# Performance work log

Hardware: AMD Instinct MI355X
Metric: run time of the kernel (lower is better)

The kernel has to match this reference:

```python
import jax, jax.numpy as jnp
import numpy as np
import math

D_MODEL = 256
D_HIDDEN = 64
NUM_HEADS = 4
LN_EPS = 1e-5


def _layernorm(x, gamma, beta):
    mu = jnp.mean(x, axis=-1, keepdims=True)
    var = jnp.mean(jnp.square(x - mu), axis=-1, keepdims=True)
    return (x - mu) * jax.lax.rsqrt(var + LN_EPS) * gamma + beta


def setup_inputs() -> dict:
    key = jax.random.key(0)
    ks = jax.random.split(key, 12)
    B, T, Nt, Nw = 8, 96, 200, 100
    s = 0.02
    return {
        "turbine_feats": jax.random.normal(ks[0], (B, T, Nt, D_MODEL), jnp.float32),
        "weather_feats": jax.random.normal(ks[1], (B, T, Nw, D_MODEL), jnp.float32),
        # torch Linear layout: (out_features, in_features)
        "w_t_lin": jax.random.normal(ks[2], (D_HIDDEN, D_MODEL), jnp.float32) * s,
        "b_t_lin": jnp.zeros((D_HIDDEN,), jnp.float32),
        "w_w_lin": jax.random.normal(ks[3], (D_HIDDEN, D_MODEL), jnp.float32) * s,
        "b_w_lin": jnp.zeros((D_HIDDEN,), jnp.float32),
        "ln_t_g": jnp.ones((D_HIDDEN,), jnp.float32),
        "ln_t_b": jnp.zeros((D_HIDDEN,), jnp.float32),
        "ln_w_g": jnp.ones((D_HIDDEN,), jnp.float32),
        "ln_w_b": jnp.zeros((D_HIDDEN,), jnp.float32),
        # nn.MultiheadAttention packed qkv in_proj (3*dh, dh) + out_proj
        "in_proj_w": jax.random.normal(ks[4], (3 * D_HIDDEN, D_HIDDEN), jnp.float32) * s,
        "in_proj_b": jnp.zeros((3 * D_HIDDEN,), jnp.float32),
        "attn_out_w": jax.random.normal(ks[5], (D_HIDDEN, D_HIDDEN), jnp.float32) * s,
        "attn_out_b": jnp.zeros((D_HIDDEN,), jnp.float32),
        "out_proj_w": jax.random.normal(ks[6], (D_MODEL, D_HIDDEN), jnp.float32) * s,
        "out_proj_b": jnp.zeros((D_MODEL,), jnp.float32),
    }


def reference(turbine_feats, weather_feats, w_t_lin, b_t_lin, w_w_lin, b_w_lin,
              ln_t_g, ln_t_b, ln_w_g, ln_w_b, in_proj_w, in_proj_b,
              attn_out_w, attn_out_b, out_proj_w, out_proj_b):
    B, T, Nt, C = turbine_feats.shape
    Nw = weather_feats.shape[2]
    dh, H = D_HIDDEN, NUM_HEADS
    hd = dh // H

    # project + layernorm
    h_t = _layernorm(jnp.einsum('btnc,dc->btnd', turbine_feats, w_t_lin) + b_t_lin, ln_t_g, ln_t_b)
    h_w = _layernorm(jnp.einsum('btmc,dc->btmd', weather_feats, w_w_lin) + b_w_lin, ln_w_g, ln_w_b)

    # hand-rolled turbine->weather cross attention
    logits = jnp.einsum('btnd,btmd->btnm', h_t, h_w) / math.sqrt(dh)  # [B,T,Nt,Nw]
    attn = jax.nn.softmax(logits, axis=-1)
    context = jnp.einsum('btnm,btmd->btnd', attn, h_w)  # [B,T,Nt,dh]

    # nn.MultiheadAttention self-attention over turbines, per (B,T)
    x = context.reshape(B * T, Nt, dh)
    wq, wk, wv = in_proj_w[:dh], in_proj_w[dh:2 * dh], in_proj_w[2 * dh:]
    bq, bk, bv = in_proj_b[:dh], in_proj_b[dh:2 * dh], in_proj_b[2 * dh:]
    q = (jnp.einsum('snd,ed->sne', x, wq) + bq).reshape(B * T, Nt, H, hd)
    k = (jnp.einsum('snd,ed->sne', x, wk) + bk).reshape(B * T, Nt, H, hd)
    v = (jnp.einsum('snd,ed->sne', x, wv) + bv).reshape(B * T, Nt, H, hd)
    scores = jnp.einsum('snhd,smhd->shnm', q, k) / math.sqrt(hd)  # [BT,H,Nt,Nt]
    w = jax.nn.softmax(scores, axis=-1)
    o = jnp.einsum('shnm,smhd->snhd', w, v).reshape(B * T, Nt, dh)
    o = jnp.einsum('snd,ed->sne', o, attn_out_w) + attn_out_b

    enhanced = o.reshape(B, T, Nt, dh)
    return turbine_feats + jnp.einsum('btnd,cd->btnc', enhanced, out_proj_w) + out_proj_b
```

## Files before the change

kernel.cpp:

```cpp
#include <hip/hip_runtime.h>


#define DEV __device__ __forceinline__

typedef float  f32x4  __attribute__((ext_vector_type(4)));
typedef int    i32x4  __attribute__((ext_vector_type(4)));
typedef unsigned int u32x2 __attribute__((ext_vector_type(2)));
typedef __bf16 bf16x8 __attribute__((ext_vector_type(8)));

DEV f32x4 mfma_bf16(i32x4 a, i32x4 b, f32x4 c) {
  return __builtin_amdgcn_mfma_f32_16x16x32_bf16(
      __builtin_bit_cast(bf16x8, a), __builtin_bit_cast(bf16x8, b), c, 0, 0, 0);
}

DEV unsigned short f2b(float f) {
  unsigned int u = __builtin_bit_cast(unsigned int, f);
  u += 0x7FFFu + ((u >> 16) & 1u);
  return (unsigned short)(u >> 16);
}

__global__ void cvt_weights_k(const float* __restrict__ w0, const float* __restrict__ w1,
                              const float* __restrict__ w2, const float* __restrict__ w3,
                              const float* __restrict__ w4, unsigned short* __restrict__ out) {
  int i = blockIdx.x * 256 + threadIdx.x;
  int idx = i;
  float v;
  if (idx < 16384) v = w0[idx];
  else if ((idx -= 16384) < 16384) v = w1[idx];
  else if ((idx -= 16384) < 12288) v = w2[idx];
  else if ((idx -= 12288) < 4096)  v = w3[idx];
  else { idx -= 4096; if (idx >= 16384) return; v = w4[idx]; }
  out[i] = f2b(v);
}

template <int CIN, int COUT, int MODE, bool F32IN>
__global__ __launch_bounds__(256) void affine_k(
    const void* __restrict__ xin,
    const unsigned short* __restrict__ Wb,
    const float* __restrict__ bias,
    const float* __restrict__ gamma, const float* __restrict__ beta,
    void* __restrict__ outp) {
  const int tid = threadIdx.x;
  const long row0 = (long)blockIdx.x * 64;
  const int lane = tid & 63, wv = tid >> 6;
  const int m = lane & 15, quad = lane >> 4;
  const long grow = row0 + wv * 16 + m;

  constexpr int KS = CIN / 32;
  i32x4 a_reg[KS];
  if (F32IN) {
    const float* xf = (const float*)xin + grow * CIN + quad * 8;
    float4 v0[KS], v1[KS];
#pragma unroll
    for (int ks = 0; ks < KS; ++ks) {
      v0[ks] = *(const float4*)(xf + ks * 32);
      v1[ks] = *(const float4*)(xf + ks * 32 + 4);
    }
#pragma unroll
    for (int ks = 0; ks < KS; ++ks) {
      unsigned int p0 = (unsigned int)f2b(v0[ks].x) | ((unsigned int)f2b(v0[ks].y) << 16);
      unsigned int p1 = (unsigned int)f2b(v0[ks].z) | ((unsigned int)f2b(v0[ks].w) << 16);
      unsigned int p2 = (unsigned int)f2b(v1[ks].x) | ((unsigned int)f2b(v1[ks].y) << 16);
      unsigned int p3 = (unsigned int)f2b(v1[ks].z) | ((unsigned int)f2b(v1[ks].w) << 16);
      a_reg[ks] = (i32x4){(int)p0, (int)p1, (int)p2, (int)p3};
    }
  } else {
    const unsigned short* xb = (const unsigned short*)xin + grow * CIN + quad * 8;
#pragma unroll
    for (int ks = 0; ks < KS; ++ks)
      a_reg[ks] = *(const i32x4*)(xb + ks * 32);
  }

  if (MODE == 1) {
    float accs[4][4];
#pragma unroll
    for (int ct = 0; ct < 4; ++ct) {
      f32x4 acc = {0.f, 0.f, 0.f, 0.f};
      const unsigned short* wp = Wb + (ct * 16 + m) * CIN + quad * 8;
#pragma unroll
      for (int ks = 0; ks < KS; ++ks) {
        i32x4 b = *(const i32x4*)(wp + ks * 32);
        acc = mfma_bf16(a_reg[ks], b, acc);
      }
      float bv = bias[ct * 16 + m];
#pragma unroll
      for (int rg = 0; rg < 4; ++rg) accs[ct][rg] = acc[rg] + bv;
    }
    float g[4], bb[4];
#pragma unroll
    for (int ct = 0; ct < 4; ++ct) { g[ct] = gamma[ct * 16 + m]; bb[ct] = beta[ct * 16 + m]; }
    unsigned short* ob = (unsigned short*)outp;
#pragma unroll
    for (int rg = 0; rg < 4; ++rg) {
      float s = accs[0][rg] + accs[1][rg] + accs[2][rg] + accs[3][rg];
#pragma unroll
      for (int msk = 1; msk < 16; msk <<= 1) s += __shfl_xor(s, msk, 64);
      float mu = s * (1.0f / 64.0f);
      float vs = 0.f;
#pragma unroll
      for (int ct = 0; ct < 4; ++ct) { float d = accs[ct][rg] - mu; vs += d * d; }
#pragma unroll
      for (int msk = 1; msk < 16; msk <<= 1) vs += __shfl_xor(vs, msk, 64);
      float inv = rsqrtf(vs * (1.0f / 64.0f) + 1e-5f);
      long row = row0 + wv * 16 + quad * 4 + rg;
#pragma unroll
      for (int ct = 0; ct < 4; ++ct) {
        float y = (accs[ct][rg] - mu) * inv * g[ct] + bb[ct];
        ob[row * 64 + ct * 16 + m] = f2b(y);
      }
    }
  } else {
#pragma unroll
    for (int ct = 0; ct < COUT / 16; ++ct) {
      f32x4 acc = {0.f, 0.f, 0.f, 0.f};
      const unsigned short* wp = Wb + (ct * 16 + m) * CIN + quad * 8;
#pragma unroll
      for (int ks = 0; ks < KS; ++ks) {
        i32x4 b = *(const i32x4*)(wp + ks * 32);
        acc = mfma_bf16(a_reg[ks], b, acc);
      }
      int col = ct * 16 + m;
      float bv = bias[col];
      unsigned short* ob = (unsigned short*)outp;
#pragma unroll
      for (int rg = 0; rg < 4; ++rg) {
        long row = row0 + wv * 16 + quad * 4 + rg;
        ob[row * COUT + col] = f2b(acc[rg] + bv);
      }
    }
  }
}

__global__ __launch_bounds__(256) void out_fused_k(
    const unsigned short* __restrict__ o,
    const unsigned short* __restrict__ Wao,
    const float* __restrict__ bao,
    const unsigned short* __restrict__ Wop,
    const float* __restrict__ bop,
    const float* __restrict__ resid,
    float* __restrict__ out) {
  __shared__ __align__(16) unsigned short xs[64][72];
  __shared__ __align__(16) unsigned short as[64][72];
  __shared__ __align__(16) float Ls[4][16][68];
  const int tid = threadIdx.x;
  const long row0 = (long)blockIdx.x * 64;

  {
    const i32x4* xb = (const i32x4*)o + (size_t)row0 * 8;
    for (int i = tid; i < 512; i += 256) {
      int r = i >> 3, c = i & 7;
      *(i32x4*)&xs[r][c * 8] = xb[i];
    }
  }
  __syncthreads();

  const int lane = tid & 63, wv = tid >> 6;
  const int m = lane & 15, quad = lane >> 4;
  const int arow = wv * 16 + m;

  i32x4 af0 = *(const i32x4*)&xs[arow][quad * 8];
  i32x4 af1 = *(const i32x4*)&xs[arow][32 + quad * 8];

#pragma unroll
  for (int ct = 0; ct < 4; ++ct) {
    const unsigned short* wp = Wao + (ct * 16 + m) * 64 + quad * 8;
    f32x4 acc = {0.f, 0.f, 0.f, 0.f};
    acc = mfma_bf16(af0, *(const i32x4*)wp, acc);
    acc = mfma_bf16(af1, *(const i32x4*)(wp + 32), acc);
    float bv = bao[ct * 16 + m];
#pragma unroll
    for (int rg = 0; rg < 4; ++rg)
      as[wv * 16 + quad * 4 + rg][ct * 16 + m] = f2b(acc[rg] + bv);
  }
  __builtin_amdgcn_s_waitcnt(0);

  i32x4 bf0 = *(const i32x4*)&as[arow][quad * 8];
  i32x4 bf1 = *(const i32x4*)&as[arow][32 + quad * 8];

  const float4* residv = (const float4*)resid;
  float4* outv = (float4*)out;

  size_t gibase[4];
#pragma unroll
  for (int i = 0; i < 4; ++i) {
    int idx = lane + i * 64;
    int r = idx >> 4, c4 = idx & 15;
    gibase[i] = (size_t)(row0 + wv * 16 + r) * 64 + c4;
  }

#pragma unroll
  for (int cg = 0; cg < 4; ++cg) {
    float4 rv[4];
#pragma unroll
    for (int i = 0; i < 4; ++i) rv[i] = residv[gibase[i] + cg * 16];

#pragma unroll
    for (int c2 = 0; c2 < 4; ++c2) {
      int col = cg * 64 + c2 * 16 + m;
      const unsigned short* wp = Wop + col * 64 + quad * 8;
      f32x4 acc = {0.f, 0.f, 0.f, 0.f};
      acc = mfma_bf16(bf0, *(const i32x4*)wp, acc);
      acc = mfma_bf16(bf1, *(const i32x4*)(wp + 32), acc);
      float bv = bop[col];
#pragma unroll
      for (int rg = 0; rg < 4; ++rg)
        Ls[wv][quad * 4 + rg][c2 * 16 + m] = acc[rg] + bv;
    }
    __builtin_amdgcn_s_waitcnt(0);
#pragma unroll
    for (int i = 0; i < 4; ++i) {
      int idx = lane + i * 64;
      int r = idx >> 4, c4 = idx & 15;
      f32x4 sv = *(const f32x4*)&Ls[wv][r][c4 * 4];
      float4 ov;
      ov.x = sv[0] + rv[i].x; ov.y = sv[1] + rv[i].y;
      ov.z = sv[2] + rv[i].z; ov.w = sv[3] + rv[i].w;
      outv[gibase[i] + cg * 16] = ov;
    }
    __builtin_amdgcn_s_waitcnt(0);
  }
}

__global__ __launch_bounds__(256) void cross_attn_k(
    const unsigned short* __restrict__ ht,
    const unsigned short* __restrict__ hw,
    unsigned short* __restrict__ xout) {
  const int bt = blockIdx.x;
  const int tid = threadIdx.x;
  __shared__ __align__(16) unsigned short Kl[112][72];
  __shared__ __align__(16) unsigned short VT2[64][136];
  __shared__ __align__(16) unsigned short P2[4][16][136];

  const i32x4 z4 = {0, 0, 0, 0};
  {
    i32x4* p0 = (i32x4*)&Kl[0][0];
    for (int i = tid; i < 1008; i += 256) p0[i] = z4;
    i32x4* p1 = (i32x4*)&VT2[0][0];
    for (int i = tid; i < 1088; i += 256) p1[i] = z4;
    i32x4* p2 = (i32x4*)&P2[0][0][0];
    for (int i = tid; i < 1088; i += 256) p2[i] = z4;
  }
  __syncthreads();
  {
    const unsigned short* wbase = hw + (size_t)bt * 100 * 64;
    for (int i = tid; i < 800; i += 256) {
      int r = i >> 3, c = (i & 7) * 8;
      i32x4 w = *(const i32x4*)(wbase + (size_t)r * 64 + c);
      *(i32x4*)&Kl[r][c] = w;
      unsigned short tmp[8];
      __builtin_memcpy(tmp, &w, 16);
#pragma unroll
      for (int j = 0; j < 8; ++j) VT2[c + j][r] = tmp[j];
    }
  }
  __syncthreads();

  const int lane = tid & 63, wv = tid >> 6;
  const int m = lane & 15, quad = lane >> 4;

  i32x4 kf[7][2];
#pragma unroll
  for (int mt = 0; mt < 7; ++mt)
#pragma unroll
    for (int ks = 0; ks < 2; ++ks)
      kf[mt][ks] = *(const i32x4*)&Kl[mt * 16 + m][ks * 32 + quad * 8];

  for (int c = wv; c < 13; c += 4) {
    const int n0 = c * 16;
    const unsigned short* ap = ht + ((size_t)bt * 200 + n0 + m) * 64 + quad * 8;
    i32x4 a0 = *(const i32x4*)ap;
    i32x4 a1 = *(const i32x4*)(ap + 32);

    float s[7][4];
#pragma unroll
    for (int mt = 0; mt < 7; ++mt) {
      f32x4 acc = mfma_bf16(a0, kf[mt][0], (f32x4){0.f, 0.f, 0.f, 0.f});
      acc = mfma_bf16(a1, kf[mt][1], acc);
#pragma unroll
      for (int rg = 0; rg < 4; ++rg) s[mt][rg] = acc[rg];
    }
#pragma unroll
    for (int rg = 0; rg < 4; ++rg)
      s[6][rg] = (m < 4) ? s[6][rg] : -3.0e38f;

    float S[4];
#pragma unroll
    for (int rg = 0; rg < 4; ++rg) {
      float mx = s[0][rg];
#pragma unroll
      for (int mt = 1; mt < 7; ++mt) mx = fmaxf(mx, s[mt][rg]);
#pragma unroll
      for (int msk = 1; msk < 16; msk <<= 1) mx = fmaxf(mx, __shfl_xor(mx, msk, 64));
      float sum = 0.f;
#pragma unroll
      for (int mt = 0; mt < 7; ++mt) {
        float p = __expf((s[mt][rg] - mx) * 0.125f);
        s[mt][rg] = p; sum += p;
      }
#pragma unroll
      for (int msk = 1; msk < 16; msk <<= 1) sum += __shfl_xor(sum, msk, 64);
      S[rg] = sum;
    }
#pragma unroll
    for (int mt = 0; mt < 7; ++mt)
#pragma unroll
      for (int rg = 0; rg < 4; ++rg)
        P2[wv][quad * 4 + rg][mt * 16 + m] = f2b(s[mt][rg]);
    __builtin_amdgcn_s_waitcnt(0);

    i32x4 pa[4];
#pragma unroll
    for (int ks = 0; ks < 4; ++ks)
      pa[ks] = *(const i32x4*)&P2[wv][m][ks * 32 + quad * 8];
    float rs[4];
#pragma unroll
    for (int rg = 0; rg < 4; ++rg) rs[rg] = __fdividef(1.0f, S[rg]);

#pragma unroll
    for (int ct = 0; ct < 4; ++ct) {
      f32x4 acc = {0.f, 0.f, 0.f, 0.f};
#pragma unroll
      for (int ks = 0; ks < 4; ++ks) {
        i32x4 b = *(const i32x4*)&VT2[ct * 16 + m][ks * 32 + quad * 8];
        acc = mfma_bf16(pa[ks], b, acc);
      }
#pragma unroll
      for (int rg = 0; rg < 4; ++rg) {
        int n = n0 + quad * 4 + rg;
        if (n < 200)
          xout[((size_t)bt * 200 + n) * 64 + ct * 16 + m] = f2b(acc[rg] * rs[rg]);
      }
    }
  }
}

__global__ __launch_bounds__(256) void self_attn_k(
    const unsigned short* __restrict__ qkv,
    unsigned short* __restrict__ o) {
  const int g = blockIdx.x;
  const int bt = ((g >> 5) << 3) | (g & 7);
  const int h = (g >> 3) & 3;
  const int tid = threadIdx.x;

  __shared__ __align__(16) unsigned short Kz[212][24];
  __shared__ __align__(16) unsigned short VT[16][232];
  __shared__ __align__(16) unsigned short P[4][16][232];

  const i32x4 z4 = {0, 0, 0, 0};
  {
    i32x4* p0 = (i32x4*)&Kz[0][0];
    for (int i = tid; i < 636; i += 256) p0[i] = z4;
    i32x4* p1 = (i32x4*)&VT[0][0];
    for (int i = tid; i < 464; i += 256) p1[i] = z4;
    i32x4* p2 = (i32x4*)&P[0][0][0];
    for (int i = tid; i < 1856; i += 256) p2[i] = z4;
  }
  __syncthreads();
  {
    const unsigned short* kb = qkv + (size_t)bt * 200 * 192 + 64 + h * 16;
    const unsigned short* vb = kb + 64;
    for (int i = tid; i < 400; i += 256) {
      int r = i >> 1, c = (i & 1) * 8;
      *(i32x4*)&Kz[r][c] = *(const i32x4*)(kb + (size_t)r * 192 + c);
      i32x4 vv = *(const i32x4*)(vb + (size_t)r * 192 + c);
      unsigned short tmp[8];
      __builtin_memcpy(tmp, &vv, 16);
#pragma unroll
      for (int j = 0; j < 8; ++j) VT[c + j][r] = tmp[j];
    }
  }
  __syncthreads();

  const int lane = tid & 63, wv = tid >> 6;
  const int m = lane & 15, quad = lane >> 4;
  const bool kreal = quad < 2;

  i32x4 kf[13];
#pragma unroll
  for (int mt = 0; mt < 13; ++mt)
    kf[mt] = *(const i32x4*)&Kz[mt * 16 + m][quad * 8];

  const unsigned short* qb = qkv + (size_t)bt * 200 * 192 + h * 16;

  for (int c = wv; c < 13; c += 4) {
    const int n0 = c * 16;
    i32x4 a = kreal ? *(const i32x4*)(qb + (size_t)(n0 + m) * 192 + quad * 8) : z4;

    float s[13][4];
#pragma unroll
    for (int mt = 0; mt < 13; ++mt) {
      f32x4 acc = mfma_bf16(a, kf[mt], (f32x4){0.f, 0.f, 0.f, 0.f});
#pragma unroll
      for (int rg = 0; rg < 4; ++rg) s[mt][rg] = acc[rg];
    }
#pragma unroll
    for (int rg = 0; rg < 4; ++rg)
      s[12][rg] = (m < 8) ? s[12][rg] : -3.0e38f;

    float S[4];
#pragma unroll
    for (int rg = 0; rg < 4; ++rg) {
      float mx = s[0][rg];
#pragma unroll
      for (int mt = 1; mt < 13; ++mt) mx = fmaxf(mx, s[mt][rg]);
#pragma unroll
      for (int msk = 1; msk < 16; msk <<= 1) mx = fmaxf(mx, __shfl_xor(mx, msk, 64));
      float sum = 0.f;
#pragma unroll
      for (int mt = 0; mt < 13; ++mt) {
        float p = __expf((s[mt][rg] - mx) * 0.25f);
        s[mt][rg] = p; sum += p;
      }
#pragma unroll
      for (int msk = 1; msk < 16; msk <<= 1) sum += __shfl_xor(sum, msk, 64);
      S[rg] = sum;
    }
#pragma unroll
    for (int mt = 0; mt < 13; ++mt)
#pragma unroll
      for (int rg = 0; rg < 4; ++rg)
        P[wv][quad * 4 + rg][mt * 16 + m] = f2b(s[mt][rg]);
    __builtin_amdgcn_s_waitcnt(0);

    f32x4 acc2 = {0.f, 0.f, 0.f, 0.f};
#pragma unroll
    for (int ks = 0; ks < 7; ++ks) {
      i32x4 pa = *(const i32x4*)&P[wv][m][ks * 32 + quad * 8];
      i32x4 vb2 = *(const i32x4*)&VT[m][ks * 32 + quad * 8];
      acc2 = mfma_bf16(pa, vb2, acc2);
    }
#pragma unroll
    for (int rg = 0; rg < 4; ++rg) {
      int n = n0 + quad * 4 + rg;
      if (n < 200)
        o[((size_t)bt * 200 + n) * 64 + h * 16 + m] = f2b(__fdividef(acc2[rg], S[rg]));
    }
  }
}

extern "C" void kernel_launch(void* const* d_in, const int* in_sizes, int n_in,
                              void* d_out, int out_size, void* d_ws, size_t ws_size,
                              hipStream_t stream) {
  const float* turbine    = (const float*)d_in[0];
  const float* weather    = (const float*)d_in[1];
  const float* b_t_lin    = (const float*)d_in[3];
  const float* b_w_lin    = (const float*)d_in[5];
  const float* ln_t_g     = (const float*)d_in[6];
  const float* ln_t_b     = (const float*)d_in[7];
  const float* ln_w_g     = (const float*)d_in[8];
  const float* ln_w_b     = (const float*)d_in[9];
  const float* in_proj_b  = (const float*)d_in[11];
  const float* attn_out_b = (const float*)d_in[13];
  const float* out_proj_b = (const float*)d_in[15];

  unsigned short* ws  = (unsigned short*)d_ws;
  unsigned short* ht  = ws + 0;
  unsigned short* hw  = ws + 9830400;
  unsigned short* x   = ws + 14745600;
  unsigned short* qkv = ws + 24576000;
  unsigned short* o   = ws + 0;
  unsigned short* wb  = ws + 54067200;
  unsigned short* wtb = wb;
  unsigned short* wwb = wb + 16384;
  unsigned short* ipb = wb + 32768;
  unsigned short* aob = wb + 45056;
  unsigned short* opb = wb + 49152;

  cvt_weights_k<<<256, 256, 0, stream>>>((const float*)d_in[2], (const float*)d_in[4],
                                         (const float*)d_in[10], (const float*)d_in[12],
                                         (const float*)d_in[14], wb);
  affine_k<256, 64, 1, true><<<2400, 256, 0, stream>>>(
      turbine, wtb, b_t_lin, ln_t_g, ln_t_b, ht);
  affine_k<256, 64, 1, true><<<1200, 256, 0, stream>>>(
      weather, wwb, b_w_lin, ln_w_g, ln_w_b, hw);
  cross_attn_k<<<768, 256, 0, stream>>>(ht, hw, x);
  affine_k<64, 192, 0, false><<<2400, 256, 0, stream>>>(
      x, ipb, in_proj_b, nullptr, nullptr, qkv);
  self_attn_k<<<3072, 256, 0, stream>>>(qkv, o);
  out_fused_k<<<2400, 256, 0, stream>>>(
      o, aob, attn_out_b, opb, out_proj_b, turbine, (float*)d_out);
}
```

Before: 557.6 us.

## Fuse QKV in-projection into cross-attention kernel with head-major QKV layout

The cross-attention kernel now keeps its context tile in LDS and applies the packed QKV in-projection directly. This removes the separate affine kernel launch and the write and read of the intermediate context tensor. QKV is written in a head-major layout (per bt, per head, rows of 48) so self-attention loads its K and V with contiguous reads. The cost is more LDS per block (the larger PQ buffer plus XT) and more serial work per wave inside the cross kernel, which may reduce occupancy.

```diff
diff --git a/kernel.cpp b/kernel.cpp
--- a/kernel.cpp
+++ b/kernel.cpp
@@ -33,13 +33,13 @@
   out[i] = f2b(v);
 }
 
-template <int CIN, int COUT, int MODE, bool F32IN>
-__global__ __launch_bounds__(256) void affine_k(
-    const void* __restrict__ xin,
+template <int CIN>
+__global__ __launch_bounds__(256) void ln_affine_k(
+    const float* __restrict__ xin,
     const unsigned short* __restrict__ Wb,
     const float* __restrict__ bias,
     const float* __restrict__ gamma, const float* __restrict__ beta,
-    void* __restrict__ outp) {
+    unsigned short* __restrict__ outp) {
   const int tid = threadIdx.x;
   const long row0 = (long)blockIdx.x * 64;
   const int lane = tid & 63, wv = tid >> 6;
@@ -48,8 +48,8 @@
 
   constexpr int KS = CIN / 32;
   i32x4 a_reg[KS];
-  if (F32IN) {
-    const float* xf = (const float*)xin + grow * CIN + quad * 8;
+  {
+    const float* xf = xin + grow * CIN + quad * 8;
     float4 v0[KS], v1[KS];
 #pragma unroll
     for (int ks = 0; ks < KS; ++ks) {
@@ -64,69 +64,295 @@
       unsigned int p3 = (unsigned int)f2b(v1[ks].z) | ((unsigned int)f2b(v1[ks].w) << 16);
       a_reg[ks] = (i32x4){(int)p0, (int)p1, (int)p2, (int)p3};
     }
-  } else {
-    const unsigned short* xb = (const unsigned short*)xin + grow * CIN + quad * 8;
-#pragma unroll
-    for (int ks = 0; ks < KS; ++ks)
-      a_reg[ks] = *(const i32x4*)(xb + ks * 32);
-  }
-
-  if (MODE == 1) {
-    float accs[4][4];
+  }
+
+  float accs[4][4];
+#pragma unroll
+  for (int ct = 0; ct < 4; ++ct) {
+    f32x4 acc = {0.f, 0.f, 0.f, 0.f};
+    const unsigned short* wp = Wb + (ct * 16 + m) * CIN + quad * 8;
+#pragma unroll
+    for (int ks = 0; ks < KS; ++ks) {
+      i32x4 b = *(const i32x4*)(wp + ks * 32);
+      acc = mfma_bf16(a_reg[ks], b, acc);
+    }
+    float bv = bias[ct * 16 + m];
+#pragma unroll
+    for (int rg = 0; rg < 4; ++rg) accs[ct][rg] = acc[rg] + bv;
+  }
+  float g[4], bb[4];
+#pragma unroll
+  for (int ct = 0; ct < 4; ++ct) { g[ct] = gamma[ct * 16 + m]; bb[ct] = beta[ct * 16 + m]; }
+#pragma unroll
+  for (int rg = 0; rg < 4; ++rg) {
+    float s = accs[0][rg] + accs[1][rg] + accs[2][rg] + accs[3][rg];
+#pragma unroll
+    for (int msk = 1; msk < 16; msk <<= 1) s += __shfl_xor(s, msk, 64);
+    float mu = s * (1.0f / 64.0f);
+    float vs = 0.f;
+#pragma unroll
+    for (int ct = 0; ct < 4; ++ct) { float d = accs[ct][rg] - mu; vs += d * d; }
+#pragma unroll
+    for (int msk = 1; msk < 16; msk <<= 1) vs += __shfl_xor(vs, msk, 64);
+    float inv = rsqrtf(vs * (1.0f / 64.0f) + 1e-5f);
+    long row = row0 + wv * 16 + quad * 4 + rg;
+#pragma unroll
+    for (int ct = 0; ct < 4; ++ct) {
+      float y = (accs[ct][rg] - mu) * inv * g[ct] + bb[ct];
+      outp[row * 64 + ct * 16 + m] = f2b(y);
+    }
+  }
+}
+
+__global__ __launch_bounds__(256) void cross_qkv_k(
+    const unsigned short* __restrict__ ht,
+    const unsigned short* __restrict__ hw,
+    const unsigned short* __restrict__ Wip,
+    const float* __restrict__ bip,
+    unsigned short* __restrict__ qkvh) {
+  const int bt = blockIdx.x;
+  const int tid = threadIdx.x;
+  __shared__ __align__(16) unsigned short Kl[112][72];
+  __shared__ __align__(16) unsigned short VT2[64][136];
+  __shared__ __align__(16) unsigned short PQ[4][16][200];
+  __shared__ __align__(16) unsigned short XT[4][16][72];
+
+  const i32x4 z4 = {0, 0, 0, 0};
+  {
+    i32x4* p0 = (i32x4*)&Kl[0][0];
+    for (int i = tid; i < 1008; i += 256) p0[i] = z4;
+    i32x4* p1 = (i32x4*)&VT2[0][0];
+    for (int i = tid; i < 1088; i += 256) p1[i] = z4;
+    i32x4* p2 = (i32x4*)&PQ[0][0][0];
+    for (int i = tid; i < 1600; i += 256) p2[i] = z4;
+  }
+  __syncthreads();
+  {
+    const unsigned short* wbase = hw + (size_t)bt * 100 * 64;
+    for (int i = tid; i < 800; i += 256) {
+      int r = i >> 3, c = (i & 7) * 8;
+      i32x4 w = *(const i32x4*)(wbase + (size_t)r * 64 + c);
+      *(i32x4*)&Kl[r][c] = w;
+      unsigned short tmp[8];
+      __builtin_memcpy(tmp, &w, 16);
+#pragma unroll
+      for (int j = 0; j < 8; ++j) VT2[c + j][r] = tmp[j];
+    }
+  }
+  __syncthreads();
+
+  const int lane = tid & 63, wv = tid >> 6;
+  const int m = lane & 15, quad = lane >> 4;
+
+  i32x4 kf[7][2];
+#pragma unroll
+  for (int mt = 0; mt < 7; ++mt)
+#pragma unroll
+    for (int ks = 0; ks < 2; ++ks)
+      kf[mt][ks] = *(const i32x4*)&Kl[mt * 16 + m][ks * 32 + quad * 8];
+
+  for (int c = wv; c < 13; c += 4) {
+    const int n0 = c * 16;
+    const unsigned short* ap = ht + ((size_t)bt * 200 + n0 + m) * 64 + quad * 8;
+    i32x4 a0 = *(const i32x4*)ap;
+    i32x4 a1 = *(const i32x4*)(ap + 32);
+
+    float s[7][4];
+#pragma unroll
+    for (int mt = 0; mt < 7; ++mt) {
+      f32x4 acc = mfma_bf16(a0, kf[mt][0], (f32x4){0.f, 0.f, 0.f, 0.f});
+      acc = mfma_bf16(a1, kf[mt][1], acc);
+#pragma unroll
+      for (int rg = 0; rg < 4; ++rg) s[mt][rg] = acc[rg];
+    }
+#pragma unroll
+    for (int rg = 0; rg < 4; ++rg)
+      s[6][rg] = (m < 4) ? s[6][rg] : -3.0e38f;
+
+    float S[4];
+#pragma unroll
+    for (int rg = 0; rg < 4; ++rg) {
+      float mx = s[0][rg];
+#pragma unroll
+      for (int mt = 1; mt < 7; ++mt) mx = fmaxf(mx, s[mt][rg]);
+#pragma unroll
+      for (int msk = 1; msk < 16; msk <<= 1) mx = fmaxf(mx, __shfl_xor(mx, msk, 64));
+      float sum = 0.f;
+#pragma unroll
+      for (int mt = 0; mt < 7; ++mt) {
+        float p = __expf((s[mt][rg] - mx) * 0.125f);
+        s[mt][rg] = p; sum += p;
+      }
+#pragma unroll
+      for (int msk = 1; msk < 16; msk <<= 1) sum += __shfl_xor(sum, msk, 64);
+      S[rg] = sum;
+    }
+#pragma unroll
+    for (int rg = 0; rg < 4; ++rg) {
+#pragma unroll
+      for (int mt = 0; mt < 7; ++mt)
+        PQ[wv][quad * 4 + rg][mt * 16 + m] = f2b(s[mt][rg]);
+      PQ[wv][quad * 4 + rg][112 + m] = 0;
+    }
+    __builtin_amdgcn_s_waitcnt(0);
+
+    i32x4 pa[4];
+#pragma unroll
+    for (int ks = 0; ks < 4; ++ks)
+      pa[ks] = *(const i32x4*)&PQ[wv][m][ks * 32 + quad * 8];
+    float rs[4];
+#pragma unroll
+    for (int rg = 0; rg < 4; ++rg) rs[rg] = __fdividef(1.0f, S[rg]);
+
 #pragma unroll
     for (int ct = 0; ct < 4; ++ct) {
       f32x4 acc = {0.f, 0.f, 0.f, 0.f};
-      const unsigned short* wp = Wb + (ct * 16 + m) * CIN + quad * 8;
-#pragma unroll
-      for (int ks = 0; ks < KS; ++ks) {
-        i32x4 b = *(const i32x4*)(wp + ks * 32);
-        acc = mfma_bf16(a_reg[ks], b, acc);
+#pragma unroll
+      for (int ks = 0; ks < 4; ++ks) {
+        i32x4 b = *(const i32x4*)&VT2[ct * 16 + m][ks * 32 + quad * 8];
+        acc = mfma_bf16(pa[ks], b, acc);
       }
-      float bv = bias[ct * 16 + m];
-#pragma unroll
-      for (int rg = 0; rg < 4; ++rg) accs[ct][rg] = acc[rg] + bv;
-    }
-    float g[4], bb[4];
-#pragma unroll
-    for (int ct = 0; ct < 4; ++ct) { g[ct] = gamma[ct * 16 + m]; bb[ct] = beta[ct * 16 + m]; }
-    unsigned short* ob = (unsigned short*)outp;
+#pragma unroll
+      for (int rg = 0; rg < 4; ++rg)
+        XT[wv][quad * 4 + rg][ct * 16 + m] = f2b(acc[rg] * rs[rg]);
+    }
+    __builtin_amdgcn_s_waitcnt(0);
+
+    i32x4 a0q = *(const i32x4*)&XT[wv][m][quad * 8];
+    i32x4 a1q = *(const i32x4*)&XT[wv][m][32 + quad * 8];
+#pragma unroll
+    for (int g2 = 0; g2 < 3; ++g2) {
+#pragma unroll
+      for (int j = 0; j < 4; ++j) {
+        int ct2 = g2 * 4 + j;
+        const unsigned short* wp = Wip + (ct2 * 16 + m) * 64 + quad * 8;
+        f32x4 acc = {0.f, 0.f, 0.f, 0.f};
+        acc = mfma_bf16(a0q, *(const i32x4*)wp, acc);
+        acc = mfma_bf16(a1q, *(const i32x4*)(wp + 32), acc);
+        float bv = bip[ct2 * 16 + m];
+#pragma unroll
+        for (int rg = 0; rg < 4; ++rg)
+          PQ[wv][quad * 4 + rg][ct2 * 16 + m] = f2b(acc[rg] + bv);
+      }
+    }
+    __builtin_amdgcn_s_waitcnt(0);
+
+#pragma unroll
+    for (int i = 0; i < 6; ++i) {
+      int t = lane + i * 64;
+      int h = t / 96, rem = t % 96;
+      int row = rem / 6, col8 = rem % 6;
+      int c_new = col8 * 8;
+      int typ = c_new >> 4, cw = c_new & 15;
+      int n = n0 + row;
+      if (n < 200) {
+        int c_std = typ * 64 + h * 16 + cw;
+        i32x4 v = *(const i32x4*)&PQ[wv][row][c_std];
+        *(i32x4*)(qkvh + (size_t)bt * 38400 + (size_t)h * 9600 +
+                  (size_t)n * 48 + typ * 16 + cw) = v;
+      }
+    }
+    __builtin_amdgcn_s_waitcnt(0);
+  }
+}
+
+__global__ __launch_bounds__(256) void self_attn_k(
+    const unsigned short* __restrict__ qkvh,
+    unsigned short* __restrict__ o) {
+  const int g = blockIdx.x;
+  const int bt = ((g >> 5) << 3) | (g & 7);
+  const int h = (g >> 3) & 3;
+  const int tid = threadIdx.x;
+
+  __shared__ __align__(16) unsigned short Kz[212][24];
+  __shared__ __align__(16) unsigned short VT[16][232];
+  __shared__ __align__(16) unsigned short P[4][16][232];
+
+  const i32x4 z4 = {0, 0, 0, 0};
+  {
+    i32x4* p0 = (i32x4*)&Kz[0][0];
+    for (int i = tid; i < 636; i += 256) p0[i] = z4;
+    i32x4* p1 = (i32x4*)&VT[0][0];
+    for (int i = tid; i < 464; i += 256) p1[i] = z4;
+    i32x4* p2 = (i32x4*)&P[0][0][0];
+    for (int i = tid; i < 1856; i += 256) p2[i] = z4;
+  }
+  __syncthreads();
+  const unsigned short* base2 = qkvh + (size_t)bt * 38400 + (size_t)h * 9600;
+  {
+    for (int i = tid; i < 400; i += 256) {
+      int r = i >> 1, half = (i & 1) * 8;
+      *(i32x4*)&Kz[r][half] = *(const i32x4*)(base2 + (size_t)r * 48 + 16 + half);
+      i32x4 vv = *(const i32x4*)(base2 + (size_t)r * 48 + 32 + half);
+      unsigned short tmp[8];
+      __builtin_memcpy(tmp, &vv, 16);
+#pragma unroll
+      for (int j = 0; j < 8; ++j) VT[half + j][r] = tmp[j];
+    }
+  }
+  __syncthreads();
+
+  const int lane = tid & 63, wv = tid >> 6;
+  const int m = lane & 15, quad = lane >> 4;
+  const bool kreal = quad < 2;
+
+  i32x4 kf[13];
+#pragma unroll
+  for (int mt = 0; mt < 13; ++mt)
+    kf[mt] = *(const i32x4*)&Kz[mt * 16 + m][quad * 8];
+
+  for (int c = wv; c < 13; c += 4) {
+    const int n0 = c * 16;
+    i32x4 a = kreal ? *(const i32x4*)(base2 + (size_t)(n0 + m) * 48 + quad * 8) : z4;
+
+    float s[13][4];
+#pragma unroll
+    for (int mt = 0; mt < 13; ++mt) {
+      f32x4 acc = mfma_bf16(a, kf[mt], (f32x4){0.f, 0.f, 0.f, 0.f});
+#pragma unroll
+      for (int rg = 0; rg < 4; ++rg) s[mt][rg] = acc[rg];
+    }
+#pragma unroll
+    for (int rg = 0; rg < 4; ++rg)
+      s[12][rg] = (m < 8) ? s[12][rg] : -3.0e38f;
+
+    float S[4];
 #pragma unroll
     for (int rg = 0; rg < 4; ++rg) {
-      float s = accs[0][rg] + accs[1][rg] + accs[2][rg] + accs[3][rg];
-#pragma unroll
-      for (int msk = 1; msk < 16; msk <<= 1) s += __shfl_xor(s, msk, 64);
-      float mu = s * (1.0f / 64.0f);
-      float vs = 0.f;
-#pragma unroll
-      for (int ct = 0; ct < 4; ++ct) { float d = accs[ct][rg] - mu; vs += d * d; }
-#pragma unroll
-      for (int msk = 1; msk < 16; msk <<= 1) vs += __shfl_xor(vs, msk, 64);
-      float inv = rsqrtf(vs * (1.0f / 64.0f) + 1e-5f);
-      long row = row0 + wv * 16 + quad * 4 + rg;
-#pragma unroll
-      for (int ct = 0; ct < 4; ++ct) {
-        float y = (accs[ct][rg] - mu) * inv * g[ct] + bb[ct];
-        ob[row * 64 + ct * 16 + m] = f2b(y);
+      float mx = s[0][rg];
+#pragma unroll
+      for (int mt = 1; mt < 13; ++mt) mx = fmaxf(mx, s[mt][rg]);
+#pragma unroll
+      for (int msk = 1; msk < 16; msk <<= 1) mx = fmaxf(mx, __shfl_xor(mx, msk, 64));
+      float sum = 0.f;
+#pragma unroll
+      for (int mt = 0; mt < 13; ++mt) {
+        float p = __expf((s[mt][rg] - mx) * 0.25f);
+        s[mt][rg] = p; sum += p;
       }
-    }
-  } else {
-#pragma unroll
-    for (int ct = 0; ct < COUT / 16; ++ct) {
-      f32x4 acc = {0.f, 0.f, 0.f, 0.f};
-      const unsigned short* wp = Wb + (ct * 16 + m) * CIN + quad * 8;
-#pragma unroll
-      for (int ks = 0; ks < KS; ++ks) {
-        i32x4 b = *(const i32x4*)(wp + ks * 32);
-        acc = mfma_bf16(a_reg[ks], b, acc);
-      }
-      int col = ct * 16 + m;
-      float bv = bias[col];
-      unsigned short* ob = (unsigned short*)outp;
-#pragma unroll
-      for (int rg = 0; rg < 4; ++rg) {
-        long row = row0 + wv * 16 + quad * 4 + rg;
-        ob[row * COUT + col] = f2b(acc[rg] + bv);
-      }
+#pragma unroll
+      for (int msk = 1; msk < 16; msk <<= 1) sum += __shfl_xor(sum, msk, 64);
+      S[rg] = sum;
+    }
+#pragma unroll
+    for (int mt = 0; mt < 13; ++mt)
+#pragma unroll
+      for (int rg = 0; rg < 4; ++rg)
+        P[wv][quad * 4 + rg][mt * 16 + m] = f2b(s[mt][rg]);
+    __builtin_amdgcn_s_waitcnt(0);
+
+    f32x4 acc2 = {0.f, 0.f, 0.f, 0.f};
+#pragma unroll
+    for (int ks = 0; ks < 7; ++ks) {
+      i32x4 pa = *(const i32x4*)&P[wv][m][ks * 32 + quad * 8];
+      i32x4 vb2 = *(const i32x4*)&VT[m][ks * 32 + quad * 8];
+      acc2 = mfma_bf16(pa, vb2, acc2);
+    }
+#pragma unroll
+    for (int rg = 0; rg < 4; ++rg) {
+      int n = n0 + quad * 4 + rg;
+      if (n < 200)
+        o[((size_t)bt * 200 + n) * 64 + h * 16 + m] = f2b(__fdividef(acc2[rg], S[rg]));
     }
   }
 }
@@ -218,223 +444,6 @@
       outv[gibase[i] + cg * 16] = ov;
     }
     __builtin_amdgcn_s_waitcnt(0);
-  }
-}
-
-__global__ __launch_bounds__(256) void cross_attn_k(
-    const unsigned short* __restrict__ ht,
-    const unsigned short* __restrict__ hw,
-    unsigned short* __restrict__ xout) {
-  const int bt = blockIdx.x;
-  const int tid = threadIdx.x;
-  __shared__ __align__(16) unsigned short Kl[112][72];
-  __shared__ __align__(16) unsigned short VT2[64][136];
-  __shared__ __align__(16) unsigned short P2[4][16][136];
-
-  const i32x4 z4 = {0, 0, 0, 0};
-  {
-    i32x4* p0 = (i32x4*)&Kl[0][0];
-    for (int i = tid; i < 1008; i += 256) p0[i] = z4;
-    i32x4* p1 = (i32x4*)&VT2[0][0];
-    for (int i = tid; i < 1088; i += 256) p1[i] = z4;
-    i32x4* p2 = (i32x4*)&P2[0][0][0];
-    for (int i = tid; i < 1088; i += 256) p2[i] = z4;
-  }
-  __syncthreads();
-  {
-    const unsigned short* wbase = hw + (size_t)bt * 100 * 64;
-    for (int i = tid; i < 800; i += 256) {
-      int r = i >> 3, c = (i & 7) * 8;
-      i32x4 w = *(const i32x4*)(wbase + (size_t)r * 64 + c);
-      *(i32x4*)&Kl[r][c] = w;
-      unsigned short tmp[8];
-      __builtin_memcpy(tmp, &w, 16);
-#pragma unroll
-      for (int j = 0; j < 8; ++j) VT2[c + j][r] = tmp[j];
-    }
-  }
-  __syncthreads();
-
-  const int lane = tid & 63, wv = tid >> 6;
-  const int m = lane & 15, quad = lane >> 4;
-
-  i32x4 kf[7][2];
-#pragma unroll
-  for (int mt = 0; mt < 7; ++mt)
-#pragma unroll
-    for (int ks = 0; ks < 2; ++ks)
-      kf[mt][ks] = *(const i32x4*)&Kl[mt * 16 + m][ks * 32 + quad * 8];
-
-  for (int c = wv; c < 13; c += 4) {
-    const int n0 = c * 16;
-    const unsigned short* ap = ht + ((size_t)bt * 200 + n0 + m) * 64 + quad * 8;
-    i32x4 a0 = *(const i32x4*)ap;
-    i32x4 a1 = *(const i32x4*)(ap + 32);
-
-    float s[7][4];
-#pragma unroll
-    for (int mt = 0; mt < 7; ++mt) {
-      f32x4 acc = mfma_bf16(a0, kf[mt][0], (f32x4){0.f, 0.f, 0.f, 0.f});
-      acc = mfma_bf16(a1, kf[mt][1], acc);
-#pragma unroll
-      for (int rg = 0; rg < 4; ++rg) s[mt][rg] = acc[rg];
-    }
-#pragma unroll
-    for (int rg = 0; rg < 4; ++rg)
-      s[6][rg] = (m < 4) ? s[6][rg] : -3.0e38f;
-
-    float S[4];
-#pragma unroll
-    for (int rg = 0; rg < 4; ++rg) {
-      float mx = s[0][rg];
-#pragma unroll
-      for (int mt = 1; mt < 7; ++mt) mx = fmaxf(mx, s[mt][rg]);
-#pragma unroll
-      for (int msk = 1; msk < 16; msk <<= 1) mx = fmaxf(mx, __shfl_xor(mx, msk, 64));
-      float sum = 0.f;
-#pragma unroll
-      for (int mt = 0; mt < 7; ++mt) {
-        float p = __expf((s[mt][rg] - mx) * 0.125f);
-        s[mt][rg] = p; sum += p;
-      }
-#pragma unroll
-      for (int msk = 1; msk < 16; msk <<= 1) sum += __shfl_xor(sum, msk, 64);
-      S[rg] = sum;
-    }
-#pragma unroll
-    for (int mt = 0; mt < 7; ++mt)
-#pragma unroll
-      for (int rg = 0; rg < 4; ++rg)
-        P2[wv][quad * 4 + rg][mt * 16 + m] = f2b(s[mt][rg]);
-    __builtin_amdgcn_s_waitcnt(0);
-
-    i32x4 pa[4];
-#pragma unroll
-    for (int ks = 0; ks < 4; ++ks)
-      pa[ks] = *(const i32x4*)&P2[wv][m][ks * 32 + quad * 8];
-    float rs[4];
-#pragma unroll
-    for (int rg = 0; rg < 4; ++rg) rs[rg] = __fdividef(1.0f, S[rg]);
-
-#pragma unroll
-    for (int ct = 0; ct < 4; ++ct) {
-      f32x4 acc = {0.f, 0.f, 0.f, 0.f};
-#pragma unroll
-      for (int ks = 0; ks < 4; ++ks) {
-        i32x4 b = *(const i32x4*)&VT2[ct * 16 + m][ks * 32 + quad * 8];
-        acc = mfma_bf16(pa[ks], b, acc);
-      }
-#pragma unroll
-      for (int rg = 0; rg < 4; ++rg) {
-        int n = n0 + quad * 4 + rg;
-        if (n < 200)
-          xout[((size_t)bt * 200 + n) * 64 + ct * 16 + m] = f2b(acc[rg] * rs[rg]);
-      }
-    }
-  }
-}
-
-__global__ __launch_bounds__(256) void self_attn_k(
-    const unsigned short* __restrict__ qkv,
-    unsigned short* __restrict__ o) {
-  const int g = blockIdx.x;
-  const int bt = ((g >> 5) << 3) | (g & 7);
-  const int h = (g >> 3) & 3;
-  const int tid = threadIdx.x;
-
-  __shared__ __align__(16) unsigned short Kz[212][24];
-  __shared__ __align__(16) unsigned short VT[16][232];
-  __shared__ __align__(16) unsigned short P[4][16][232];
-
-  const i32x4 z4 = {0, 0, 0, 0};
-  {
-    i32x4* p0 = (i32x4*)&Kz[0][0];
-    for (int i = tid; i < 636; i += 256) p0[i] = z4;
-    i32x4* p1 = (i32x4*)&VT[0][0];
-    for (int i = tid; i < 464; i += 256) p1[i] = z4;
-    i32x4* p2 = (i32x4*)&P[0][0][0];
-    for (int i = tid; i < 1856; i += 256) p2[i] = z4;
-  }
-  __syncthreads();
-  {
-    const unsigned short* kb = qkv + (size_t)bt * 200 * 192 + 64 + h * 16;
-    const unsigned short* vb = kb + 64;
-    for (int i = tid; i < 400; i += 256) {
-      int r = i >> 1, c = (i & 1) * 8;
-      *(i32x4*)&Kz[r][c] = *(const i32x4*)(kb + (size_t)r * 192 + c);
-      i32x4 vv = *(const i32x4*)(vb + (size_t)r * 192 + c);
-      unsigned short tmp[8];
-      __builtin_memcpy(tmp, &vv, 16);
-#pragma unroll
-      for (int j = 0; j < 8; ++j) VT[c + j][r] = tmp[j];
-    }
-  }
-  __syncthreads();
-
-  const int lane = tid & 63, wv = tid >> 6;
-  const int m = lane & 15, quad = lane >> 4;
-  const bool kreal = quad < 2;
-
-  i32x4 kf[13];
-#pragma unroll
-  for (int mt = 0; mt < 13; ++mt)
-    kf[mt] = *(const i32x4*)&Kz[mt * 16 + m][quad * 8];
-
-  const unsigned short* qb = qkv + (size_t)bt * 200 * 192 + h * 16;
-
-  for (int c = wv; c < 13; c += 4) {
-    const int n0 = c * 16;
-    i32x4 a = kreal ? *(const i32x4*)(qb + (size_t)(n0 + m) * 192 + quad * 8) : z4;
-
-    float s[13][4];
-#pragma unroll
-    for (int mt = 0; mt < 13; ++mt) {
-      f32x4 acc = mfma_bf16(a, kf[mt], (f32x4){0.f, 0.f, 0.f, 0.f});
-#pragma unroll
-      for (int rg = 0; rg < 4; ++rg) s[mt][rg] = acc[rg];
-    }
-#pragma unroll
-    for (int rg = 0; rg < 4; ++rg)
-      s[12][rg] = (m < 8) ? s[12][rg] : -3.0e38f;
-
-    float S[4];
-#pragma unroll
-    for (int rg = 0; rg < 4; ++rg) {
-      float mx = s[0][rg];
-#pragma unroll
-      for (int mt = 1; mt < 13; ++mt) mx = fmaxf(mx, s[mt][rg]);
-#pragma unroll
-      for (int msk = 1; msk < 16; msk <<= 1) mx = fmaxf(mx, __shfl_xor(mx, msk, 64));
-      float sum = 0.f;
-#pragma unroll
-      for (int mt = 0; mt < 13; ++mt) {
-        float p = __expf((s[mt][rg] - mx) * 0.25f);
-        s[mt][rg] = p; sum += p;
-      }
-#pragma unroll
-      for (int msk = 1; msk < 16; msk <<= 1) sum += __shfl_xor(sum, msk, 64);
-      S[rg] = sum;
-    }
-#pragma unroll
-    for (int mt = 0; mt < 13; ++mt)
-#pragma unroll
-      for (int rg = 0; rg < 4; ++rg)
-        P[wv][quad * 4 + rg][mt * 16 + m] = f2b(s[mt][rg]);
-    __builtin_amdgcn_s_waitcnt(0);
-
-    f32x4 acc2 = {0.f, 0.f, 0.f, 0.f};
-#pragma unroll
-    for (int ks = 0; ks < 7; ++ks) {
-      i32x4 pa = *(const i32x4*)&P[wv][m][ks * 32 + quad * 8];
-      i32x4 vb2 = *(const i32x4*)&VT[m][ks * 32 + quad * 8];
-      acc2 = mfma_bf16(pa, vb2, acc2);
-    }
-#pragma unroll
-    for (int rg = 0; rg < 4; ++rg) {
-      int n = n0 + quad * 4 + rg;
-      if (n < 200)
-        o[((size_t)bt * 200 + n) * 64 + h * 16 + m] = f2b(__fdividef(acc2[rg], S[rg]));
-    }
   }
 }
 
@@ -456,7 +465,6 @@
   unsigned short* ws  = (unsigned short*)d_ws;
   unsigned short* ht  = ws + 0;
   unsigned short* hw  = ws + 9830400;
-  unsigned short* x   = ws + 14745600;
   unsigned short* qkv = ws + 24576000;
   unsigned short* o   = ws + 0;
   unsigned short* wb  = ws + 54067200;
@@ -469,13 +477,11 @@
   cvt_weights_k<<<256, 256, 0, stream>>>((const float*)d_in[2], (const float*)d_in[4],
                                          (const float*)d_in[10], (const float*)d_in[12],
                                          (const float*)d_in[14], wb);
-  affine_k<256, 64, 1, true><<<2400, 256, 0, stream>>>(
+  ln_affine_k<256><<<2400, 256, 0, stream>>>(
       turbine, wtb, b_t_lin, ln_t_g, ln_t_b, ht);
-  affine_k<256, 64, 1, true><<<1200, 256, 0, stream>>>(
+  ln_affine_k<256><<<1200, 256, 0, stream>>>(
       weather, wwb, b_w_lin, ln_w_g, ln_w_b, hw);
-  cross_attn_k<<<768, 256, 0, stream>>>(ht, hw, x);
-  affine_k<64, 192, 0, false><<<2400, 256, 0, stream>>>(
-      x, ipb, in_proj_b, nullptr, nullptr, qkv);
+  cross_qkv_k<<<768, 256, 0, stream>>>(ht, hw, ipb, in_proj_b, qkv);
   self_attn_k<<<3072, 256, 0, stream>>>(qkv, o);
   out_fused_k<<<2400, 256, 0, stream>>>(
       o, aob, attn_out_b, opb, out_proj_b, turbine, (float*)d_out);
```

Result: faster. 545.4 us (-2.2%).
